# Kernel optimization log

Measured on AMD Instinct MI355X. Metric: run time of the kernel, lower is better.

The kernel has to match this reference:

```python
import jax, jax.numpy as jnp
import numpy as np

B, L, D, V = 2, 512, 512, 32000
TRAIN_FRAC = 0.01
LOSS_WEIGHTS = (1.0, 0.25)  # (forward branch, backward_ar_loss_weight)


def _make_pairs():
    # cartesian_prod(arange(L), arange(L)) filtered by bi - fi >= 2, then random subsample
    fi_g, bi_g = np.meshgrid(np.arange(L), np.arange(L), indexing='ij')
    fi_all, bi_all = fi_g.ravel(), bi_g.ravel()
    valid = (bi_all - fi_all) >= 2
    fi_all, bi_all = fi_all[valid], bi_all[valid]
    num_pairs = fi_all.shape[0]
    n_sub = max(int(num_pairs * TRAIN_FRAC), 1)
    perm = np.random.default_rng(0).permutation(num_pairs)[:n_sub]
    return jnp.asarray(fi_all[perm], jnp.int32), jnp.asarray(bi_all[perm], jnp.int32)


def setup_inputs() -> dict:
    key = jax.random.key(0)
    k_fe, k_be, k_seq, k_w1, k_w2 = jax.random.split(key, 5)
    fi, bi = _make_pairs()  # [N], N = 1303
    return {
        'forward_embeds': jax.random.normal(k_fe, (B, L, D), jnp.float32),
        'backward_embeds': jax.random.normal(k_be, (B, L, D), jnp.float32),
        'seq': jax.random.randint(k_seq, (B, L), 0, V, dtype=jnp.int32),
        'fi': fi,
        'bi': bi,
        'w1': jax.random.normal(k_w1, (2 * D, D), jnp.float32) * 0.02,
        'b1': jnp.zeros((D,), jnp.float32),
        'w2': jax.random.normal(k_w2, (D, 2 * V), jnp.float32) * 0.02,
        'b2': jnp.zeros((2 * V,), jnp.float32),
    }


def reference(forward_embeds, backward_embeds, seq, fi, bi, w1, b1, w2, b2):
    # gather fwd/bwd embeddings at the (fi, bi) pair indices and concat: [B, N, 2D]
    fb_embeds = jnp.concatenate([forward_embeds[:, fi], backward_embeds[:, bi]], axis=-1)
    # text head: Linear(2D->D) -> LeakyReLU(0.01) -> Linear(D->2V)
    h = jax.nn.leaky_relu(jnp.einsum('bne,ed->bnd', fb_embeds, w1) + b1)
    logits = jnp.einsum('bnd,dv->bnv', h, w2) + b2  # [B, N, 2V]
    n = logits.shape[1]
    # (fb l) layout: first V classes = forward branch, last V = backward branch
    logp = jax.nn.log_softmax(logits.reshape(B, n, 2, V), axis=-1)  # [B, N, 2, V]
    # NOTE: source computes labels_fi = fi + 1 but actually indexes seq at fi/bi
    labels = jnp.stack([seq[:, fi], seq[:, bi]], axis=-1)  # [B, N, 2]
    nll = -jnp.take_along_axis(logp, labels[..., None], axis=-1)[..., 0]  # [B, N, 2]
    w = jnp.asarray(LOSS_WEIGHTS, logits.dtype)  # per-branch loss weights
    return (nll * w).mean()
```

## Files before the change

kernel.cpp:

```cpp
#include <hip/hip_runtime.h>


typedef __bf16 bf16x8 __attribute__((ext_vector_type(8)));
typedef __bf16 bf16x4 __attribute__((ext_vector_type(4)));
typedef float f32x4  __attribute__((ext_vector_type(4)));

#define MFMA16(a, b, c) __builtin_amdgcn_mfma_f32_16x16x32_bf16(a, b, c, 0, 0, 0)

static constexpr int Bsz   = 2;
static constexpr int L     = 512;
static constexpr int D     = 512;
static constexpr int V     = 32000;
static constexpr int K1    = 2 * D;
static constexpr int N1    = D;
static constexpr int K2    = D;
static constexpr int N2    = 2 * V;
static constexpr int NSTRIP = N2 / 64;

__device__ __host__ inline size_t apack_chunk(int panel, int ks, int mi) {
    return (((size_t)panel * 16 + ks) * 4 + mi) * 512;
}

__global__ void gather_cast_kernel(const float* __restrict__ fwd,
                                   const float* __restrict__ bwd,
                                   const int* __restrict__ fi,
                                   const int* __restrict__ bi,
                                   const int* __restrict__ seq,
                                   __bf16* __restrict__ A1,
                                   int* __restrict__ labcol,
                                   int N, int M, int Mpad) {
    int t = blockIdx.x * 256 + threadIdx.x;
    if (t < Mpad * 2) {
        int m = t >> 1, br = t & 1;
        if (m >= M) labcol[t] = -1;
        else {
            int b = m / N, n = m - b * N;
            int tok = br ? seq[b * L + bi[n]] : seq[b * L + fi[n]];
            labcol[t] = br * V + tok;
        }
    }
    int total = Mpad * (K1 / 8);
    if (t >= total) return;
    int m  = t >> 7;
    int c8 = (t & 127) * 8;
    bf16x8 out;
    if (m < M) {
        int b = m / N;
        int n = m - b * N;
        const float* src;
        if (c8 < D) src = fwd + ((size_t)(b * L + fi[n])) * D + c8;
        else        src = bwd + ((size_t)(b * L + bi[n])) * D + (c8 - D);
        float4 v0 = *(const float4*)(src);
        float4 v1 = *(const float4*)(src + 4);
        out[0] = (__bf16)v0.x; out[1] = (__bf16)v0.y;
        out[2] = (__bf16)v0.z; out[3] = (__bf16)v0.w;
        out[4] = (__bf16)v1.x; out[5] = (__bf16)v1.y;
        out[6] = (__bf16)v1.z; out[7] = (__bf16)v1.w;
    } else {
        for (int j = 0; j < 8; j++) out[j] = (__bf16)0.0f;
    }
    *(bf16x8*)(A1 + (size_t)m * K1 + c8) = out;
}

__global__ void transpose_cast_kernel(const float* __restrict__ src,
                                      __bf16* __restrict__ dst,
                                      int K, int Nn) {
    __shared__ __align__(16) __bf16 tile[64][68];
    int t  = threadIdx.x;
    int tx = t & 15, ty = t >> 4;
    int n0 = blockIdx.x * 64, k0 = blockIdx.y * 64;
    for (int i = 0; i < 4; i++) {
        int k = k0 + ty + 16 * i;
        float4 v = *(const float4*)(src + (size_t)k * Nn + n0 + tx * 4);
        tile[tx * 4 + 0][ty + 16 * i] = (__bf16)v.x;
        tile[tx * 4 + 1][ty + 16 * i] = (__bf16)v.y;
        tile[tx * 4 + 2][ty + 16 * i] = (__bf16)v.z;
        tile[tx * 4 + 3][ty + 16 * i] = (__bf16)v.w;
    }
    __syncthreads();
    for (int i = 0; i < 4; i++) {
        int n = n0 + ty + 16 * i;
        bf16x4 o;
        o[0] = tile[ty + 16 * i][tx * 4 + 0];
        o[1] = tile[ty + 16 * i][tx * 4 + 1];
        o[2] = tile[ty + 16 * i][tx * 4 + 2];
        o[3] = tile[ty + 16 * i][tx * 4 + 3];
        *(bf16x4*)(dst + (size_t)n * K + k0 + tx * 4) = o;
    }
}

__global__ __launch_bounds__(256) void gemm1_kernel(
        const __bf16* __restrict__ A, const __bf16* __restrict__ Bt,
        const float* __restrict__ bias, __bf16* __restrict__ Apack, int K) {
    __shared__ __align__(16) __bf16 At[128][40];
    __shared__ __align__(16) __bf16 Bl[128][40];
    __shared__ __align__(16) __bf16 Cld[128][136];
    const int t = threadIdx.x;
    const int by = blockIdx.y, bx = blockIdx.x;
    const int m0 = by * 128, n0 = bx * 128;
    const int srow = t >> 2, schunk = (t & 3) * 8;
    const int wave = t >> 6, lane = t & 63;
    const int wrow = (wave >> 1) * 64, wcol = (wave & 1) * 64;
    const int q = lane >> 4, ln = lane & 15;

    f32x4 acc[4][4] = {};
    for (int k0 = 0; k0 < K; k0 += 32) {
        __syncthreads();
        *(bf16x8*)&At[srow][schunk]      = *(const bf16x8*)(A  + (size_t)(m0 + srow)      * K + k0 + schunk);
        *(bf16x8*)&At[srow + 64][schunk] = *(const bf16x8*)(A  + (size_t)(m0 + srow + 64) * K + k0 + schunk);
        *(bf16x8*)&Bl[srow][schunk]      = *(const bf16x8*)(Bt + (size_t)(n0 + srow)      * K + k0 + schunk);
        *(bf16x8*)&Bl[srow + 64][schunk] = *(const bf16x8*)(Bt + (size_t)(n0 + srow + 64) * K + k0 + schunk);
        __syncthreads();
        bf16x8 af[4], bfr[4];
        for (int i = 0; i < 4; i++) af[i]  = *(const bf16x8*)&At[wrow + i * 16 + ln][q * 8];
        for (int i = 0; i < 4; i++) bfr[i] = *(const bf16x8*)&Bl[wcol + i * 16 + ln][q * 8];
        for (int mi = 0; mi < 4; mi++)
            for (int ni = 0; ni < 4; ni++)
                acc[mi][ni] = MFMA16(af[mi], bfr[ni], acc[mi][ni]);
    }
    for (int ni = 0; ni < 4; ni++) {
        int gcol = n0 + wcol + ni * 16 + ln;
        float bv = bias[gcol];
        for (int mi = 0; mi < 4; mi++)
            for (int r = 0; r < 4; r++) {
                float v = acc[mi][ni][r] + bv;
                v = v > 0.0f ? v : 0.01f * v;
                Cld[wrow + mi * 16 + q * 4 + r][wcol + ni * 16 + ln] = (__bf16)v;
            }
    }
    __syncthreads();
    for (int i = 0; i < 8; i++) {
        int c   = wave + 4 * i;
        int pl  = c >> 4, ksl = (c >> 2) & 3, mi = c & 3;
        int row = pl * 64 + mi * 16 + (lane & 15);
        int col = ksl * 32 + (lane >> 4) * 8;
        bf16x8 v = *(const bf16x8*)&Cld[row][col];
        size_t base = apack_chunk(2 * by + pl, 4 * bx + ksl, mi);
        *(bf16x8*)(Apack + base + lane * 8) = v;
    }
}

__global__ __launch_bounds__(512, 4) void gemm2_kernel(
        const __bf16* __restrict__ Apack, const float* __restrict__ w2,
        const float* __restrict__ b2, const int* __restrict__ labcol,
        float* __restrict__ partial, float* __restrict__ lab, int Mpad) {
    __shared__ __align__(16) __bf16 Bp[64 * 512];
    const int t = threadIdx.x;
    const int strip = blockIdx.x;
    const int c0 = strip * 64;
    const int branch = (c0 >= V) ? 1 : 0;

    {
        const int col = t & 63;
        const int ni = col >> 4, lncol = col & 15;
        const int kb0 = (t >> 6) * 8;
        for (int r = 0; r < 8; r++) {
            int kb = kb0 + r * 64;
            int ks = kb >> 5, qk = (kb >> 3) & 3;
            float v[8];
#pragma unroll
            for (int j = 0; j < 8; j++)
                v[j] = __builtin_nontemporal_load(w2 + (size_t)(kb + j) * N2 + c0 + col);
            bf16x8 o;
#pragma unroll
            for (int j = 0; j < 8; j++) o[j] = (__bf16)v[j];
            *(bf16x8*)&Bp[(size_t)(((ks * 4 + ni) * 64 + qk * 16 + lncol)) * 8] = o;
        }
    }
    __syncthreads();

    const int wave = t >> 6, lane = t & 63;
    const int q = lane >> 4, ln = lane & 15;

    float bvn[4];
#pragma unroll
    for (int ni = 0; ni < 4; ni++) bvn[ni] = b2[c0 + ni * 16 + ln];

    const int npanels = Mpad >> 6;
    for (int p = wave; p < npanels; p += 8) {
        const __bf16* base = Apack + apack_chunk(p, 0, 0) + lane * 8;

        f32x4 acc[4][4] = {};
        bf16x8 afc[4], afn[4];
#pragma unroll
        for (int mi = 0; mi < 4; mi++)
            afc[mi] = *(const bf16x8*)(base + mi * 512);
#pragma unroll 1
        for (int ks = 0; ks < 16; ks++) {
            if (ks < 15) {
#pragma unroll
                for (int mi = 0; mi < 4; mi++)
                    afn[mi] = *(const bf16x8*)(base + (size_t)(ks + 1) * 2048 + mi * 512);
            }
            bf16x8 bf[4];
#pragma unroll
            for (int ni = 0; ni < 4; ni++)
                bf[ni] = *(const bf16x8*)&Bp[(size_t)(ks * 4 + ni) * 512 + lane * 8];
#pragma unroll
            for (int mi = 0; mi < 4; mi++)
#pragma unroll
                for (int ni = 0; ni < 4; ni++)
                    acc[mi][ni] = MFMA16(afc[mi], bf[ni], acc[mi][ni]);
#pragma unroll
            for (int mi = 0; mi < 4; mi++) afc[mi] = afn[mi];
        }

        int lc[4][4];
#pragma unroll
        for (int mi = 0; mi < 4; mi++)
#pragma unroll
            for (int r = 0; r < 4; r++)
                lc[mi][r] = labcol[(p * 64 + mi * 16 + q * 4 + r) * 2 + branch];

        float rowsum[4][4];
#pragma unroll
        for (int mi = 0; mi < 4; mi++)
#pragma unroll
            for (int r = 0; r < 4; r++) rowsum[mi][r] = 0.0f;

#pragma unroll
        for (int ni = 0; ni < 4; ni++) {
            const int gcol = c0 + ni * 16 + ln;
            const float bv = bvn[ni];
#pragma unroll
            for (int mi = 0; mi < 4; mi++)
#pragma unroll
                for (int r = 0; r < 4; r++) {
                    float v = acc[mi][ni][r] + bv;
                    rowsum[mi][r] += __expf(v);
                    if (gcol == lc[mi][r]) {
                        int gm = p * 64 + mi * 16 + q * 4 + r;
                        lab[gm * 2 + branch] = v;
                    }
                }
        }
#pragma unroll
        for (int mi = 0; mi < 4; mi++)
#pragma unroll
            for (int r = 0; r < 4; r++) {
                float s = rowsum[mi][r];
                s += __shfl_xor(s, 1);
                s += __shfl_xor(s, 2);
                s += __shfl_xor(s, 4);
                s += __shfl_xor(s, 8);
                rowsum[mi][r] = s;
            }
        float mine = 0.0f;
        const int srcl = ((lane >> 2) & 3) * 16;
#pragma unroll
        for (int mi2 = 0; mi2 < 4; mi2++)
#pragma unroll
            for (int r2 = 0; r2 < 4; r2++) {
                float tv = __shfl(rowsum[mi2][r2], srcl);
                if ((lane >> 4) == mi2 && (lane & 3) == r2) mine = tv;
            }
        partial[(size_t)strip * Mpad + p * 64 + lane] = mine;
    }
}

__global__ void reduce_sumexp_kernel(const float* __restrict__ partial,
                                     float* __restrict__ sumexp, int Mpad) {
    int t = blockIdx.x * 256 + threadIdx.x;
    if (t >= Mpad * 2) return;
    int br = t / Mpad, m = t - br * Mpad;
    int s0 = br * (NSTRIP / 2), s1 = s0 + NSTRIP / 2;
    float s = 0.0f;
#pragma unroll 4
    for (int si = s0; si < s1; si++)
        s += partial[(size_t)si * Mpad + m];
    sumexp[m * 2 + br] = s;
}

__global__ void final_reduce_kernel(const float* __restrict__ sumexp,
                                    const float* __restrict__ lab,
                                    float* __restrict__ out, int M) {
    __shared__ float red[4];
    float acc = 0.0f;
    for (int m = threadIdx.x; m < M; m += 256) {
        float nf = logf(sumexp[m * 2 + 0]) - lab[m * 2 + 0];
        float nb = logf(sumexp[m * 2 + 1]) - lab[m * 2 + 1];
        acc += nf + 0.25f * nb;
    }
    acc += __shfl_xor(acc, 32);
    acc += __shfl_xor(acc, 16);
    acc += __shfl_xor(acc, 8);
    acc += __shfl_xor(acc, 4);
    acc += __shfl_xor(acc, 2);
    acc += __shfl_xor(acc, 1);
    int wv = threadIdx.x >> 6, ln = threadIdx.x & 63;
    if (ln == 0) red[wv] = acc;
    __syncthreads();
    if (threadIdx.x == 0)
        out[0] = (red[0] + red[1] + red[2] + red[3]) / (float)(2 * M);
}

extern "C" void kernel_launch(void* const* d_in, const int* in_sizes, int n_in,
                              void* d_out, int out_size, void* d_ws, size_t ws_size,
                              hipStream_t stream) {
    const float* fwd = (const float*)d_in[0];
    const float* bwd = (const float*)d_in[1];
    const int*   seq = (const int*)d_in[2];
    const int*   fi  = (const int*)d_in[3];
    const int*   bi  = (const int*)d_in[4];
    const float* w1  = (const float*)d_in[5];
    const float* b1  = (const float*)d_in[6];
    const float* w2  = (const float*)d_in[7];
    const float* b2  = (const float*)d_in[8];
    float* out = (float*)d_out;

    const int N    = in_sizes[3];
    const int M    = Bsz * N;
    const int Mpad = ((M + 255) / 256) * 256;

    char* ws = (char*)d_ws;
    __bf16* A1    = (__bf16*)(ws);
    __bf16* W1T   = (__bf16*)(ws + (size_t)Mpad * K1 * 2);
    __bf16* Apack = (__bf16*)((char*)W1T + (size_t)N1 * K1 * 2);
    float*  partial = (float*)((char*)Apack + (size_t)Mpad * N1 * 2);
    float*  sumexp  = (float*)((char*)partial + (size_t)NSTRIP * Mpad * 4);
    float*  lab     = (float*)((char*)sumexp + (size_t)Mpad * 2 * 4);
    int*    labcol  = (int*)((char*)lab + (size_t)Mpad * 2 * 4);

    {
        int total = Mpad * (K1 / 8);
        gather_cast_kernel<<<(total + 255) / 256, 256, 0, stream>>>(
            fwd, bwd, fi, bi, seq, A1, labcol, N, M, Mpad);
    }
    transpose_cast_kernel<<<dim3(N1 / 64, K1 / 64), 256, 0, stream>>>(w1, W1T, K1, N1);
    gemm1_kernel<<<dim3(N1 / 128, Mpad / 128), 256, 0, stream>>>(A1, W1T, b1, Apack, K1);
    gemm2_kernel<<<NSTRIP, 512, 0, stream>>>(Apack, w2, b2, labcol, partial, lab, Mpad);
    reduce_sumexp_kernel<<<(Mpad * 2 + 255) / 256, 256, 0, stream>>>(partial, sumexp, Mpad);
    final_reduce_kernel<<<1, 256, 0, stream>>>(sumexp, lab, out, M);
}
```

Before: 441.8 us.

## Fuse prep and final kernels, unroll gemm2 k-loop, cheapen softmax epilogue

Merges the gather/cast and W1 transpose into one launch, and merges the sumexp reduction with the final NLL reduction using an atomicAdd into a zeroed output. In gemm2 it unrolls the k-loop by two with ping-pong A fragments and computes exp via exp2 with a fused multiply-add. The label-logit capture moves into a separate branch taken only when a label column falls in the strip. This cuts launch count and epilogue ALU work, but adds a memset and an atomic, which makes the float summation order nondeterministic.

```diff
diff --git a/kernel.cpp b/kernel.cpp
--- a/kernel.cpp
+++ b/kernel.cpp
@@ -16,19 +16,49 @@
 static constexpr int K2    = D;
 static constexpr int N2    = 2 * V;
 static constexpr int NSTRIP = N2 / 64;
+static constexpr float LOG2E = 1.44269504088896340736f;
 
 __device__ __host__ inline size_t apack_chunk(int panel, int ks, int mi) {
     return (((size_t)panel * 16 + ks) * 4 + mi) * 512;
 }
 
-__global__ void gather_cast_kernel(const float* __restrict__ fwd,
-                                   const float* __restrict__ bwd,
-                                   const int* __restrict__ fi,
-                                   const int* __restrict__ bi,
-                                   const int* __restrict__ seq,
-                                   __bf16* __restrict__ A1,
-                                   int* __restrict__ labcol,
-                                   int N, int M, int Mpad) {
+__global__ void prep_kernel(const float* __restrict__ fwd,
+                            const float* __restrict__ bwd,
+                            const int* __restrict__ fi,
+                            const int* __restrict__ bi,
+                            const int* __restrict__ seq,
+                            const float* __restrict__ w1,
+                            __bf16* __restrict__ A1,
+                            __bf16* __restrict__ W1T,
+                            int* __restrict__ labcol,
+                            int N, int M, int Mpad, int G1) {
+    __shared__ __align__(16) __bf16 tile[64][68];
+    if ((int)blockIdx.x >= G1) {
+        int bid = blockIdx.x - G1;
+        int bx = bid & 7, by = bid >> 3;
+        int t  = threadIdx.x;
+        int tx = t & 15, ty = t >> 4;
+        int n0 = bx * 64, k0 = by * 64;
+        for (int i = 0; i < 4; i++) {
+            int k = k0 + ty + 16 * i;
+            float4 v = *(const float4*)(w1 + (size_t)k * N1 + n0 + tx * 4);
+            tile[tx * 4 + 0][ty + 16 * i] = (__bf16)v.x;
+            tile[tx * 4 + 1][ty + 16 * i] = (__bf16)v.y;
+            tile[tx * 4 + 2][ty + 16 * i] = (__bf16)v.z;
+            tile[tx * 4 + 3][ty + 16 * i] = (__bf16)v.w;
+        }
+        __syncthreads();
+        for (int i = 0; i < 4; i++) {
+            int n = n0 + ty + 16 * i;
+            bf16x4 o;
+            o[0] = tile[ty + 16 * i][tx * 4 + 0];
+            o[1] = tile[ty + 16 * i][tx * 4 + 1];
+            o[2] = tile[ty + 16 * i][tx * 4 + 2];
+            o[3] = tile[ty + 16 * i][tx * 4 + 3];
+            *(bf16x4*)(W1T + (size_t)n * K1 + k0 + tx * 4) = o;
+        }
+        return;
+    }
     int t = blockIdx.x * 256 + threadIdx.x;
     if (t < Mpad * 2) {
         int m = t >> 1, br = t & 1;
@@ -62,33 +92,6 @@
     *(bf16x8*)(A1 + (size_t)m * K1 + c8) = out;
 }
 
-__global__ void transpose_cast_kernel(const float* __restrict__ src,
-                                      __bf16* __restrict__ dst,
-                                      int K, int Nn) {
-    __shared__ __align__(16) __bf16 tile[64][68];
-    int t  = threadIdx.x;
-    int tx = t & 15, ty = t >> 4;
-    int n0 = blockIdx.x * 64, k0 = blockIdx.y * 64;
-    for (int i = 0; i < 4; i++) {
-        int k = k0 + ty + 16 * i;
-        float4 v = *(const float4*)(src + (size_t)k * Nn + n0 + tx * 4);
-        tile[tx * 4 + 0][ty + 16 * i] = (__bf16)v.x;
-        tile[tx * 4 + 1][ty + 16 * i] = (__bf16)v.y;
-        tile[tx * 4 + 2][ty + 16 * i] = (__bf16)v.z;
-        tile[tx * 4 + 3][ty + 16 * i] = (__bf16)v.w;
-    }
-    __syncthreads();
-    for (int i = 0; i < 4; i++) {
-        int n = n0 + ty + 16 * i;
-        bf16x4 o;
-        o[0] = tile[ty + 16 * i][tx * 4 + 0];
-        o[1] = tile[ty + 16 * i][tx * 4 + 1];
-        o[2] = tile[ty + 16 * i][tx * 4 + 2];
-        o[3] = tile[ty + 16 * i][tx * 4 + 3];
-        *(bf16x4*)(dst + (size_t)n * K + k0 + tx * 4) = o;
-    }
-}
-
 __global__ __launch_bounds__(256) void gemm1_kernel(
         const __bf16* __restrict__ A, const __bf16* __restrict__ Bt,
         const float* __restrict__ bias, __bf16* __restrict__ Apack, int K) {
@@ -172,67 +175,114 @@
     const int wave = t >> 6, lane = t & 63;
     const int q = lane >> 4, ln = lane & 15;
 
-    float bvn[4];
-#pragma unroll
-    for (int ni = 0; ni < 4; ni++) bvn[ni] = b2[c0 + ni * 16 + ln];
+    float bvn[4], bvl2[4];
+#pragma unroll
+    for (int ni = 0; ni < 4; ni++) {
+        bvn[ni] = b2[c0 + ni * 16 + ln];
+        bvl2[ni] = bvn[ni] * LOG2E;
+    }
 
     const int npanels = Mpad >> 6;
     for (int p = wave; p < npanels; p += 8) {
         const __bf16* base = Apack + apack_chunk(p, 0, 0) + lane * 8;
 
         f32x4 acc[4][4] = {};
-        bf16x8 afc[4], afn[4];
-#pragma unroll
-        for (int mi = 0; mi < 4; mi++)
-            afc[mi] = *(const bf16x8*)(base + mi * 512);
+        bf16x8 afA[4], afB[4];
+#pragma unroll
+        for (int mi = 0; mi < 4; mi++)
+            afA[mi] = *(const bf16x8*)(base + mi * 512);
 #pragma unroll 1
-        for (int ks = 0; ks < 16; ks++) {
-            if (ks < 15) {
+        for (int ks = 0; ks < 14; ks += 2) {
+#pragma unroll
+            for (int mi = 0; mi < 4; mi++)
+                afB[mi] = *(const bf16x8*)(base + (size_t)(ks + 1) * 2048 + mi * 512);
+            {
+                bf16x8 bf0[4];
+#pragma unroll
+                for (int ni = 0; ni < 4; ni++)
+                    bf0[ni] = *(const bf16x8*)&Bp[(size_t)(ks * 4 + ni) * 512 + lane * 8];
 #pragma unroll
                 for (int mi = 0; mi < 4; mi++)
-                    afn[mi] = *(const bf16x8*)(base + (size_t)(ks + 1) * 2048 + mi * 512);
-            }
-            bf16x8 bf[4];
+#pragma unroll
+                    for (int ni = 0; ni < 4; ni++)
+                        acc[mi][ni] = MFMA16(afA[mi], bf0[ni], acc[mi][ni]);
+            }
+#pragma unroll
+            for (int mi = 0; mi < 4; mi++)
+                afA[mi] = *(const bf16x8*)(base + (size_t)(ks + 2) * 2048 + mi * 512);
+            {
+                bf16x8 bf1[4];
+#pragma unroll
+                for (int ni = 0; ni < 4; ni++)
+                    bf1[ni] = *(const bf16x8*)&Bp[(size_t)((ks + 1) * 4 + ni) * 512 + lane * 8];
+#pragma unroll
+                for (int mi = 0; mi < 4; mi++)
+#pragma unroll
+                    for (int ni = 0; ni < 4; ni++)
+                        acc[mi][ni] = MFMA16(afB[mi], bf1[ni], acc[mi][ni]);
+            }
+        }
+        {
+#pragma unroll
+            for (int mi = 0; mi < 4; mi++)
+                afB[mi] = *(const bf16x8*)(base + (size_t)15 * 2048 + mi * 512);
+            bf16x8 bf0[4];
 #pragma unroll
             for (int ni = 0; ni < 4; ni++)
-                bf[ni] = *(const bf16x8*)&Bp[(size_t)(ks * 4 + ni) * 512 + lane * 8];
+                bf0[ni] = *(const bf16x8*)&Bp[(size_t)(14 * 4 + ni) * 512 + lane * 8];
 #pragma unroll
             for (int mi = 0; mi < 4; mi++)
 #pragma unroll
                 for (int ni = 0; ni < 4; ni++)
-                    acc[mi][ni] = MFMA16(afc[mi], bf[ni], acc[mi][ni]);
-#pragma unroll
-            for (int mi = 0; mi < 4; mi++) afc[mi] = afn[mi];
+                    acc[mi][ni] = MFMA16(afA[mi], bf0[ni], acc[mi][ni]);
+            bf16x8 bf1[4];
+#pragma unroll
+            for (int ni = 0; ni < 4; ni++)
+                bf1[ni] = *(const bf16x8*)&Bp[(size_t)(15 * 4 + ni) * 512 + lane * 8];
+#pragma unroll
+            for (int mi = 0; mi < 4; mi++)
+#pragma unroll
+                for (int ni = 0; ni < 4; ni++)
+                    acc[mi][ni] = MFMA16(afB[mi], bf1[ni], acc[mi][ni]);
         }
 
         int lc[4][4];
-#pragma unroll
-        for (int mi = 0; mi < 4; mi++)
-#pragma unroll
-            for (int r = 0; r < 4; r++)
+        bool hit = false;
+#pragma unroll
+        for (int mi = 0; mi < 4; mi++)
+#pragma unroll
+            for (int r = 0; r < 4; r++) {
                 lc[mi][r] = labcol[(p * 64 + mi * 16 + q * 4 + r) * 2 + branch];
+                hit |= ((unsigned)(lc[mi][r] - c0) < 64u);
+            }
+        if (__any(hit)) {
+#pragma unroll
+            for (int ni = 0; ni < 4; ni++) {
+                const int gcol = c0 + ni * 16 + ln;
+#pragma unroll
+                for (int mi = 0; mi < 4; mi++)
+#pragma unroll
+                    for (int r = 0; r < 4; r++)
+                        if (gcol == lc[mi][r]) {
+                            int gm = p * 64 + mi * 16 + q * 4 + r;
+                            lab[gm * 2 + branch] = acc[mi][ni][r] + bvn[ni];
+                        }
+            }
+        }
 
         float rowsum[4][4];
 #pragma unroll
         for (int mi = 0; mi < 4; mi++)
 #pragma unroll
             for (int r = 0; r < 4; r++) rowsum[mi][r] = 0.0f;
-
 #pragma unroll
         for (int ni = 0; ni < 4; ni++) {
-            const int gcol = c0 + ni * 16 + ln;
-            const float bv = bvn[ni];
-#pragma unroll
-            for (int mi = 0; mi < 4; mi++)
-#pragma unroll
-                for (int r = 0; r < 4; r++) {
-                    float v = acc[mi][ni][r] + bv;
-                    rowsum[mi][r] += __expf(v);
-                    if (gcol == lc[mi][r]) {
-                        int gm = p * 64 + mi * 16 + q * 4 + r;
-                        lab[gm * 2 + branch] = v;
-                    }
-                }
+            const float bl2 = bvl2[ni];
+#pragma unroll
+            for (int mi = 0; mi < 4; mi++)
+#pragma unroll
+                for (int r = 0; r < 4; r++)
+                    rowsum[mi][r] += __builtin_exp2f(__builtin_fmaf(acc[mi][ni][r], LOG2E, bl2));
         }
 #pragma unroll
         for (int mi = 0; mi < 4; mi++)
@@ -258,28 +308,22 @@
     }
 }
 
-__global__ void reduce_sumexp_kernel(const float* __restrict__ partial,
-                                     float* __restrict__ sumexp, int Mpad) {
+__global__ void final_kernel(const float* __restrict__ partial,
+                             const float* __restrict__ lab,
+                             float* __restrict__ out, int M, int Mpad) {
+    __shared__ float red[4];
     int t = blockIdx.x * 256 + threadIdx.x;
-    if (t >= Mpad * 2) return;
-    int br = t / Mpad, m = t - br * Mpad;
-    int s0 = br * (NSTRIP / 2), s1 = s0 + NSTRIP / 2;
-    float s = 0.0f;
+    float acc = 0.0f;
+    if (t < 2 * M) {
+        int br = (t >= M) ? 1 : 0;
+        int m = t - br * M;
+        int s0 = br * (NSTRIP / 2), s1 = s0 + NSTRIP / 2;
+        float s = 0.0f;
 #pragma unroll 4
-    for (int si = s0; si < s1; si++)
-        s += partial[(size_t)si * Mpad + m];
-    sumexp[m * 2 + br] = s;
-}
-
-__global__ void final_reduce_kernel(const float* __restrict__ sumexp,
-                                    const float* __restrict__ lab,
-                                    float* __restrict__ out, int M) {
-    __shared__ float red[4];
-    float acc = 0.0f;
-    for (int m = threadIdx.x; m < M; m += 256) {
-        float nf = logf(sumexp[m * 2 + 0]) - lab[m * 2 + 0];
-        float nb = logf(sumexp[m * 2 + 1]) - lab[m * 2 + 1];
-        acc += nf + 0.25f * nb;
+        for (int si = s0; si < s1; si++)
+            s += partial[(size_t)si * Mpad + m];
+        float nll = logf(s) - lab[m * 2 + br];
+        acc = (br ? 0.25f : 1.0f) * nll;
     }
     acc += __shfl_xor(acc, 32);
     acc += __shfl_xor(acc, 16);
@@ -291,7 +335,7 @@
     if (ln == 0) red[wv] = acc;
     __syncthreads();
     if (threadIdx.x == 0)
-        out[0] = (red[0] + red[1] + red[2] + red[3]) / (float)(2 * M);
+        atomicAdd(out, (red[0] + red[1] + red[2] + red[3]) / (float)(2 * M));
 }
 
 extern "C" void kernel_launch(void* const* d_in, const int* in_sizes, int n_in,
@@ -317,18 +361,16 @@
     __bf16* W1T   = (__bf16*)(ws + (size_t)Mpad * K1 * 2);
     __bf16* Apack = (__bf16*)((char*)W1T + (size_t)N1 * K1 * 2);
     float*  partial = (float*)((char*)Apack + (size_t)Mpad * N1 * 2);
-    float*  sumexp  = (float*)((char*)partial + (size_t)NSTRIP * Mpad * 4);
-    float*  lab     = (float*)((char*)sumexp + (size_t)Mpad * 2 * 4);
+    float*  lab     = (float*)((char*)partial + (size_t)NSTRIP * Mpad * 4);
     int*    labcol  = (int*)((char*)lab + (size_t)Mpad * 2 * 4);
 
     {
-        int total = Mpad * (K1 / 8);
-        gather_cast_kernel<<<(total + 255) / 256, 256, 0, stream>>>(
-            fwd, bwd, fi, bi, seq, A1, labcol, N, M, Mpad);
-    }
-    transpose_cast_kernel<<<dim3(N1 / 64, K1 / 64), 256, 0, stream>>>(w1, W1T, K1, N1);
+        int G1 = Mpad * (K1 / 8) / 256;
+        prep_kernel<<<G1 + 128, 256, 0, stream>>>(
+            fwd, bwd, fi, bi, seq, w1, A1, W1T, labcol, N, M, Mpad, G1);
+    }
+    hipMemsetAsync(out, 0, sizeof(float), stream);
     gemm1_kernel<<<dim3(N1 / 128, Mpad / 128), 256, 0, stream>>>(A1, W1T, b1, Apack, K1);
     gemm2_kernel<<<NSTRIP, 512, 0, stream>>>(Apack, w2, b2, labcol, partial, lab, Mpad);
-    reduce_sumexp_kernel<<<(Mpad * 2 + 255) / 256, 256, 0, stream>>>(partial, sumexp, Mpad);
-    final_reduce_kernel<<<1, 256, 0, stream>>>(sumexp, lab, out, M);
-}
+    final_kernel<<<(2 * M + 255) / 256, 256, 0, stream>>>(partial, lab, out, M, Mpad);
+}
```

Measured after the change: 496.3 us. +12.4%, slower.

## Merge prep kernels, streamline softmax epilogue, fuse final reductions with atomics

Applied to the files above, without the earlier changes.

Folds the w1 transpose-cast into the gather kernel as extra blocks and merges the sumexp reduction with the final loss reduction into one multi-block kernel that accumulates through atomicAdd, which needs a memset of the output. In the GEMM2 epilogue the exp is rewritten as exp2 of an FMA with a pre-scaled bias, and the label-match check runs only when a wave's labels fall in the strip. Labels are stored per branch so each lane reads one label. The intent is fewer launches and less epilogue ALU and compare work, at the cost of a non-deterministic atomic summation order.

```diff
diff --git a/kernel.cpp b/kernel.cpp
--- a/kernel.cpp
+++ b/kernel.cpp
@@ -16,27 +16,57 @@
 static constexpr int K2    = D;
 static constexpr int N2    = 2 * V;
 static constexpr int NSTRIP = N2 / 64;
+static constexpr float LOG2E = 1.44269504088896340736f;
 
 __device__ __host__ inline size_t apack_chunk(int panel, int ks, int mi) {
     return (((size_t)panel * 16 + ks) * 4 + mi) * 512;
 }
 
-__global__ void gather_cast_kernel(const float* __restrict__ fwd,
-                                   const float* __restrict__ bwd,
-                                   const int* __restrict__ fi,
-                                   const int* __restrict__ bi,
-                                   const int* __restrict__ seq,
-                                   __bf16* __restrict__ A1,
-                                   int* __restrict__ labcol,
-                                   int N, int M, int Mpad) {
+__global__ void prep_kernel(const float* __restrict__ fwd,
+                            const float* __restrict__ bwd,
+                            const int* __restrict__ fi,
+                            const int* __restrict__ bi,
+                            const int* __restrict__ seq,
+                            const float* __restrict__ w1,
+                            __bf16* __restrict__ A1,
+                            __bf16* __restrict__ W1T,
+                            int* __restrict__ labcol,
+                            int N, int M, int Mpad, int G1) {
+    __shared__ __align__(16) __bf16 tile[64][68];
+    if ((int)blockIdx.x >= G1) {
+        int bid = blockIdx.x - G1;
+        int bx = bid & 7, by = bid >> 3;
+        int t  = threadIdx.x;
+        int tx = t & 15, ty = t >> 4;
+        int n0 = bx * 64, k0 = by * 64;
+        for (int i = 0; i < 4; i++) {
+            int k = k0 + ty + 16 * i;
+            float4 v = *(const float4*)(w1 + (size_t)k * N1 + n0 + tx * 4);
+            tile[tx * 4 + 0][ty + 16 * i] = (__bf16)v.x;
+            tile[tx * 4 + 1][ty + 16 * i] = (__bf16)v.y;
+            tile[tx * 4 + 2][ty + 16 * i] = (__bf16)v.z;
+            tile[tx * 4 + 3][ty + 16 * i] = (__bf16)v.w;
+        }
+        __syncthreads();
+        for (int i = 0; i < 4; i++) {
+            int n = n0 + ty + 16 * i;
+            bf16x4 o;
+            o[0] = tile[ty + 16 * i][tx * 4 + 0];
+            o[1] = tile[ty + 16 * i][tx * 4 + 1];
+            o[2] = tile[ty + 16 * i][tx * 4 + 2];
+            o[3] = tile[ty + 16 * i][tx * 4 + 3];
+            *(bf16x4*)(W1T + (size_t)n * K1 + k0 + tx * 4) = o;
+        }
+        return;
+    }
     int t = blockIdx.x * 256 + threadIdx.x;
     if (t < Mpad * 2) {
         int m = t >> 1, br = t & 1;
-        if (m >= M) labcol[t] = -1;
+        if (m >= M) labcol[br * Mpad + m] = -1;
         else {
             int b = m / N, n = m - b * N;
             int tok = br ? seq[b * L + bi[n]] : seq[b * L + fi[n]];
-            labcol[t] = br * V + tok;
+            labcol[br * Mpad + m] = br * V + tok;
         }
     }
     int total = Mpad * (K1 / 8);
@@ -62,33 +92,6 @@
     *(bf16x8*)(A1 + (size_t)m * K1 + c8) = out;
 }
 
-__global__ void transpose_cast_kernel(const float* __restrict__ src,
-                                      __bf16* __restrict__ dst,
-                                      int K, int Nn) {
-    __shared__ __align__(16) __bf16 tile[64][68];
-    int t  = threadIdx.x;
-    int tx = t & 15, ty = t >> 4;
-    int n0 = blockIdx.x * 64, k0 = blockIdx.y * 64;
-    for (int i = 0; i < 4; i++) {
-        int k = k0 + ty + 16 * i;
-        float4 v = *(const float4*)(src + (size_t)k * Nn + n0 + tx * 4);
-        tile[tx * 4 + 0][ty + 16 * i] = (__bf16)v.x;
-        tile[tx * 4 + 1][ty + 16 * i] = (__bf16)v.y;
-        tile[tx * 4 + 2][ty + 16 * i] = (__bf16)v.z;
-        tile[tx * 4 + 3][ty + 16 * i] = (__bf16)v.w;
-    }
-    __syncthreads();
-    for (int i = 0; i < 4; i++) {
-        int n = n0 + ty + 16 * i;
-        bf16x4 o;
-        o[0] = tile[ty + 16 * i][tx * 4 + 0];
-        o[1] = tile[ty + 16 * i][tx * 4 + 1];
-        o[2] = tile[ty + 16 * i][tx * 4 + 2];
-        o[3] = tile[ty + 16 * i][tx * 4 + 3];
-        *(bf16x4*)(dst + (size_t)n * K + k0 + tx * 4) = o;
-    }
-}
-
 __global__ __launch_bounds__(256) void gemm1_kernel(
         const __bf16* __restrict__ A, const __bf16* __restrict__ Bt,
         const float* __restrict__ bias, __bf16* __restrict__ Apack, int K) {
@@ -171,10 +174,11 @@
 
     const int wave = t >> 6, lane = t & 63;
     const int q = lane >> 4, ln = lane & 15;
-
-    float bvn[4];
-#pragma unroll
-    for (int ni = 0; ni < 4; ni++) bvn[ni] = b2[c0 + ni * 16 + ln];
+    const int* labB = labcol + branch * Mpad;
+
+    float bvl2[4];
+#pragma unroll
+    for (int ni = 0; ni < 4; ni++) bvl2[ni] = b2[c0 + ni * 16 + ln] * LOG2E;
 
     const int npanels = Mpad >> 6;
     for (int p = wave; p < npanels; p += 8) {
@@ -205,35 +209,40 @@
             for (int mi = 0; mi < 4; mi++) afc[mi] = afn[mi];
         }
 
-        int lc[4][4];
-#pragma unroll
-        for (int mi = 0; mi < 4; mi++)
-#pragma unroll
-            for (int r = 0; r < 4; r++)
-                lc[mi][r] = labcol[(p * 64 + mi * 16 + q * 4 + r) * 2 + branch];
+        int myl = labB[p * 64 + lane];
 
         float rowsum[4][4];
 #pragma unroll
         for (int mi = 0; mi < 4; mi++)
 #pragma unroll
             for (int r = 0; r < 4; r++) rowsum[mi][r] = 0.0f;
-
 #pragma unroll
         for (int ni = 0; ni < 4; ni++) {
-            const int gcol = c0 + ni * 16 + ln;
-            const float bv = bvn[ni];
+            const float bl2 = bvl2[ni];
 #pragma unroll
             for (int mi = 0; mi < 4; mi++)
 #pragma unroll
-                for (int r = 0; r < 4; r++) {
-                    float v = acc[mi][ni][r] + bv;
-                    rowsum[mi][r] += __expf(v);
-                    if (gcol == lc[mi][r]) {
-                        int gm = p * 64 + mi * 16 + q * 4 + r;
-                        lab[gm * 2 + branch] = v;
+                for (int r = 0; r < 4; r++)
+                    rowsum[mi][r] += __builtin_exp2f(__builtin_fmaf(acc[mi][ni][r], LOG2E, bl2));
+        }
+
+        if (__any((unsigned)(myl - c0) < 64u)) {
+#pragma unroll
+            for (int ni = 0; ni < 4; ni++) {
+                const int gcol = c0 + ni * 16 + ln;
+                const float bv = b2[gcol];
+#pragma unroll
+                for (int mi = 0; mi < 4; mi++)
+#pragma unroll
+                    for (int r = 0; r < 4; r++) {
+                        int row = p * 64 + mi * 16 + q * 4 + r;
+                        if (gcol == labB[row]) {
+                            lab[row * 2 + branch] = acc[mi][ni][r] + bv;
+                        }
                     }
-                }
-        }
+            }
+        }
+
 #pragma unroll
         for (int mi = 0; mi < 4; mi++)
 #pragma unroll
@@ -258,40 +267,34 @@
     }
 }
 
-__global__ void reduce_sumexp_kernel(const float* __restrict__ partial,
-                                     float* __restrict__ sumexp, int Mpad) {
-    int t = blockIdx.x * 256 + threadIdx.x;
-    if (t >= Mpad * 2) return;
-    int br = t / Mpad, m = t - br * Mpad;
-    int s0 = br * (NSTRIP / 2), s1 = s0 + NSTRIP / 2;
+__global__ __launch_bounds__(256) void final_kernel(
+        const float* __restrict__ partial, const float* __restrict__ lab,
+        float* __restrict__ out, int M, int Mpad) {
+    __shared__ float red[4][64];
+    const int br = blockIdx.x & 1;
+    const int m0 = (blockIdx.x >> 1) * 64;
+    const int wave = threadIdx.x >> 6, lane = threadIdx.x & 63;
+    const int s0 = br * (NSTRIP / 2) + wave * (NSTRIP / 8);
     float s = 0.0f;
-#pragma unroll 4
-    for (int si = s0; si < s1; si++)
-        s += partial[(size_t)si * Mpad + m];
-    sumexp[m * 2 + br] = s;
-}
-
-__global__ void final_reduce_kernel(const float* __restrict__ sumexp,
-                                    const float* __restrict__ lab,
-                                    float* __restrict__ out, int M) {
-    __shared__ float red[4];
-    float acc = 0.0f;
-    for (int m = threadIdx.x; m < M; m += 256) {
-        float nf = logf(sumexp[m * 2 + 0]) - lab[m * 2 + 0];
-        float nb = logf(sumexp[m * 2 + 1]) - lab[m * 2 + 1];
-        acc += nf + 0.25f * nb;
-    }
-    acc += __shfl_xor(acc, 32);
-    acc += __shfl_xor(acc, 16);
-    acc += __shfl_xor(acc, 8);
-    acc += __shfl_xor(acc, 4);
-    acc += __shfl_xor(acc, 2);
-    acc += __shfl_xor(acc, 1);
-    int wv = threadIdx.x >> 6, ln = threadIdx.x & 63;
-    if (ln == 0) red[wv] = acc;
+#pragma unroll 5
+    for (int i = 0; i < NSTRIP / 8; i++)
+        s += partial[(size_t)(s0 + i) * Mpad + m0 + lane];
+    red[wave][lane] = s;
     __syncthreads();
-    if (threadIdx.x == 0)
-        out[0] = (red[0] + red[1] + red[2] + red[3]) / (float)(2 * M);
+    if (wave == 0) {
+        float tot = red[0][lane] + red[1][lane] + red[2][lane] + red[3][lane];
+        int m = m0 + lane;
+        float acc = 0.0f;
+        if (m < M)
+            acc = (br ? 0.25f : 1.0f) * (logf(tot) - lab[m * 2 + br]);
+        acc += __shfl_xor(acc, 32);
+        acc += __shfl_xor(acc, 16);
+        acc += __shfl_xor(acc, 8);
+        acc += __shfl_xor(acc, 4);
+        acc += __shfl_xor(acc, 2);
+        acc += __shfl_xor(acc, 1);
+        if (lane == 0) atomicAdd(out, acc / (float)(2 * M));
+    }
 }
 
 extern "C" void kernel_launch(void* const* d_in, const int* in_sizes, int n_in,
@@ -317,18 +320,16 @@
     __bf16* W1T   = (__bf16*)(ws + (size_t)Mpad * K1 * 2);
     __bf16* Apack = (__bf16*)((char*)W1T + (size_t)N1 * K1 * 2);
     float*  partial = (float*)((char*)Apack + (size_t)Mpad * N1 * 2);
-    float*  sumexp  = (float*)((char*)partial + (size_t)NSTRIP * Mpad * 4);
-    float*  lab     = (float*)((char*)sumexp + (size_t)Mpad * 2 * 4);
+    float*  lab     = (float*)((char*)partial + (size_t)NSTRIP * Mpad * 4);
     int*    labcol  = (int*)((char*)lab + (size_t)Mpad * 2 * 4);
 
     {
-        int total = Mpad * (K1 / 8);
-        gather_cast_kernel<<<(total + 255) / 256, 256, 0, stream>>>(
-            fwd, bwd, fi, bi, seq, A1, labcol, N, M, Mpad);
-    }
-    transpose_cast_kernel<<<dim3(N1 / 64, K1 / 64), 256, 0, stream>>>(w1, W1T, K1, N1);
+        int G1 = Mpad * (K1 / 8) / 256;
+        prep_kernel<<<G1 + 128, 256, 0, stream>>>(
+            fwd, bwd, fi, bi, seq, w1, A1, W1T, labcol, N, M, Mpad, G1);
+    }
+    hipMemsetAsync(out, 0, sizeof(float), stream);
     gemm1_kernel<<<dim3(N1 / 128, Mpad / 128), 256, 0, stream>>>(A1, W1T, b1, Apack, K1);
     gemm2_kernel<<<NSTRIP, 512, 0, stream>>>(Apack, w2, b2, labcol, partial, lab, Mpad);
-    reduce_sumexp_kernel<<<(Mpad * 2 + 255) / 256, 256, 0, stream>>>(partial, sumexp, Mpad);
-    final_reduce_kernel<<<1, 256, 0, stream>>>(sumexp, lab, out, M);
-}
+    final_kernel<<<(Mpad / 64) * 2, 256, 0, stream>>>(partial, lab, out, M, Mpad);
+}
```

Result: no change. 442.6 us (+0.2%).
